# Kernel tuning notes

Measured on AMD Instinct MI355X. Metric: run time of the kernel, lower is better.

Reference implementation:

```python
import jax, jax.numpy as jnp
import numpy as np

N_NODES = 100000
N_EDGES = 3200000
N_GRAPHS = 256
DIMS = [38, 64, 32, 16]


def setup_inputs() -> dict:
    key = jax.random.key(0)
    ks = jax.random.split(key, 16)
    x = jax.random.normal(ks[0], (N_NODES, DIMS[0]), dtype=jnp.float32)
    edge_index = jax.random.randint(ks[1], (2, N_EDGES), 0, N_NODES, dtype=jnp.int64)
    batch_vec = jnp.sort(jax.random.randint(ks[2], (N_NODES,), 0, N_GRAPHS, dtype=jnp.int64))
    inp = {"x": x, "edge_index": edge_index, "batch_vec": batch_vec}
    # Per layer l: W_rel [out,in] (with bias b [out]), W_root [out,in] (no bias)
    ki = 3
    for l in range(3):
        din, dout = DIMS[l], DIMS[l + 1]
        s = 1.0 / np.sqrt(din)
        inp[f"W_rel{l}"] = jax.random.uniform(ks[ki], (dout, din), minval=-s, maxval=s, dtype=jnp.float32); ki += 1
        inp[f"b{l}"] = jax.random.uniform(ks[ki], (dout,), minval=-s, maxval=s, dtype=jnp.float32); ki += 1
        inp[f"W_root{l}"] = jax.random.uniform(ks[ki], (dout, din), minval=-s, maxval=s, dtype=jnp.float32); ki += 1
    return inp


def _graph_conv(x, src, dst, W_rel, b, W_root):
    # sum_{j -> i} x_j, then linear (equivalent to summing transformed messages)
    agg = jax.ops.segment_sum(x[src], dst, num_segments=N_NODES)  # [N, din]
    return agg @ W_rel.T + b + x @ W_root.T


def reference(x, edge_index, batch_vec, W_rel0, b0, W_root0, W_rel1, b1, W_root1, W_rel2, b2, W_root2):
    src, dst = edge_index[0], edge_index[1]
    h = jnp.tanh(_graph_conv(x, src, dst, W_rel0, b0, W_root0))
    h = jnp.tanh(_graph_conv(h, src, dst, W_rel1, b1, W_root1))
    h = _graph_conv(h, src, dst, W_rel2, b2, W_root2)
    # global mean pool over graphs
    sums = jax.ops.segment_sum(h, batch_vec, num_segments=N_GRAPHS)  # [G, 16]
    counts = jax.ops.segment_sum(jnp.ones((N_NODES,), dtype=h.dtype), batch_vec, num_segments=N_GRAPHS)
    pooled = sums / jnp.maximum(counts, 1.0)[:, None]
    return jnp.tanh(pooled)
```

## Files before the change

kernel.cpp:

```cpp
#include <hip/hip_runtime.h>
#include <math.h>

#define N_NODES  100000
#define N_EDGES  3200000
#define N_GRAPHS 256


#define BSHIFT 8
#define NB 391
#define CAP 10240
#define NBLK 320
#define EPB ((N_EDGES + NBLK - 1) / NBLK)

typedef _Float16 f16;
typedef _Float16 f16x2 __attribute__((ext_vector_type(2)));

__device__ __forceinline__ float fast_tanh(float x) {
    x = fminf(20.f, fmaxf(-20.f, x));
    float e = __expf(2.f * x);
    return (e - 1.f) / (e + 1.f);
}

__device__ __forceinline__ unsigned int pack_bf2(float a, float b) {
    unsigned int ua = __float_as_uint(a);
    unsigned int ub = __float_as_uint(b);
    ua += 0x7fffu + ((ua >> 16) & 1u);
    ub += 0x7fffu + ((ub >> 16) & 1u);
    return (ua >> 16) | (ub & 0xffff0000u);
}

__device__ __forceinline__ f16x2 u2h(unsigned int u) { union { unsigned int u; f16x2 h; } c; c.u = u; return c.h; }
__device__ __forceinline__ unsigned int h2u(f16x2 h) { union { unsigned int u; f16x2 h; } c; c.h = h; return c.u; }
__device__ __forceinline__ unsigned int mkh2(float a, float b) {
    f16x2 v; v.x = (f16)a; v.y = (f16)b; return h2u(v);
}

__device__ __forceinline__ float fdot2f(f16x2 a, f16x2 b, float c) {
#if __has_builtin(__builtin_amdgcn_fdot2)
    return __builtin_amdgcn_fdot2(a, b, c, false);
#else
    return c + (float)a.x * (float)b.x + (float)a.y * (float)b.y;
#endif
}

__global__ __launch_bounds__(256) void k_scatter2(const int* __restrict__ src,
                                                  const int* __restrict__ dst,
                                                  int* __restrict__ bucket_cnt,
                                                  int* __restrict__ ebuf) {
    __shared__ int hist[NB];
    __shared__ int base[NB];
    __shared__ int cur[NB];
    int tid = threadIdx.x, b = blockIdx.x;
    for (int i = tid; i < NB; i += 256) { hist[i] = 0; cur[i] = 0; }
    __syncthreads();
    int lo = b * EPB, hi = min(lo + EPB, N_EDGES);
    for (int e = lo + tid; e < hi; e += 256)
        atomicAdd(&hist[((unsigned int)dst[e]) >> BSHIFT], 1);
    __syncthreads();
    for (int i = tid; i < NB; i += 256) {
        int c = hist[i];
        base[i] = (c > 0) ? atomicAdd(&bucket_cnt[i], c) : 0;
    }
    __syncthreads();
    for (int e = lo + tid; e < hi; e += 256) {
        int d = dst[e];
        int bin = d >> BSHIFT;
        int r = base[bin] + atomicAdd(&cur[bin], 1);
        if (r < CAP) ebuf[bin * CAP + r] = src[e] | ((d & 255) << 17);
    }
}

__global__ __launch_bounds__(256) void k_bucket_csr2(const int* __restrict__ bucket_cnt,
                                                     int* __restrict__ ebuf,
                                                     int* __restrict__ rowptr,
                                                     int* __restrict__ rowend) {
    __shared__ int stage[CAP];
    __shared__ int cnt[256];
    __shared__ int off[256];
    __shared__ int cur[256];
    __shared__ int sscan[256];
    int b = blockIdx.x;
    int tid = threadIdx.x;
    int base = b * CAP;
    int n = min(bucket_cnt[b], CAP);
    cnt[tid] = 0;
    cur[tid] = 0;
    __syncthreads();
    for (int j = tid; j < n; j += 256) {
        int w = ebuf[base + j];
        stage[j] = w;
        atomicAdd(&cnt[((unsigned int)w) >> 17], 1);
    }
    __syncthreads();
    int v = cnt[tid];
    int val = v;
    sscan[tid] = val;
    __syncthreads();
#pragma unroll
    for (int o = 1; o < 256; o <<= 1) {
        int t = (tid >= o) ? sscan[tid - o] : 0;
        __syncthreads();
        val += t;
        sscan[tid] = val;
        __syncthreads();
    }
    int excl = val - v;
    off[tid] = excl;
    int node = (b << BSHIFT) + tid;
    if (node < N_NODES) {
        rowptr[node] = base + excl;
        rowend[node] = base + val;
    }
    __syncthreads();
    for (int j = tid; j < n; j += 256) {
        int w = stage[j];
        int dl = ((unsigned int)w) >> 17;
        int r = atomicAdd(&cur[dl], 1);
        ebuf[base + off[dl] + r] = w & 0x1FFFF;
    }
}

__global__ __launch_bounds__(256) void k_cast_slices(const float* __restrict__ in,
                                                     unsigned int* __restrict__ s0,
                                                     unsigned int* __restrict__ s1,
                                                     unsigned int* __restrict__ s2) {
    int i = blockIdx.x * 256 + threadIdx.x;
    if (i >= N_NODES * 19) return;
    int n = i / 19;
    int p = i - n * 19;
    float2 v = ((const float2*)in)[i];
    unsigned int w = pack_bf2(v.x, v.y);
    if (p < 8)       s0[n * 8 + p] = w;
    else if (p < 16) s1[n * 8 + p - 8] = w;
    else             s2[n * 3 + p - 16] = w;
}

template<int DIM2, int ASTRIDE, int OFF>
__global__ __launch_bounds__(256) void k_gather_slice(const unsigned int* __restrict__ feat,
                                                      const int* __restrict__ rowptr,
                                                      const int* __restrict__ rowend,
                                                      const int* __restrict__ elist,
                                                      float* __restrict__ agg) {
    int idx = blockIdx.x * 256 + threadIdx.x;
    if (idx >= N_NODES * DIM2) return;
    int n = idx / DIM2;
    int p = idx - n * DIM2;
    int j = rowptr[n];
    int e = rowend[n];
    float a0 = 0.f, a1 = 0.f;
    for (; j + 3 < e; j += 4) {
        int s0 = elist[j];
        int s1 = elist[j + 1];
        int s2 = elist[j + 2];
        int s3 = elist[j + 3];
        unsigned int w0 = feat[s0 * DIM2 + p];
        unsigned int w1 = feat[s1 * DIM2 + p];
        unsigned int w2 = feat[s2 * DIM2 + p];
        unsigned int w3 = feat[s3 * DIM2 + p];
        a0 += __uint_as_float(w0 << 16);
        a1 += __uint_as_float(w0 & 0xffff0000u);
        a0 += __uint_as_float(w1 << 16);
        a1 += __uint_as_float(w1 & 0xffff0000u);
        a0 += __uint_as_float(w2 << 16);
        a1 += __uint_as_float(w2 & 0xffff0000u);
        a0 += __uint_as_float(w3 << 16);
        a1 += __uint_as_float(w3 & 0xffff0000u);
    }
    for (; j < e; ++j) {
        unsigned int w = feat[elist[j] * DIM2 + p];
        a0 += __uint_as_float(w << 16);
        a1 += __uint_as_float(w & 0xffff0000u);
    }
    agg[n * ASTRIDE + OFF + 2 * p]     = a0;
    agg[n * ASTRIDE + OFF + 2 * p + 1] = a1;
}

__global__ __launch_bounds__(256) void k_fused0(const float* __restrict__ agg,
                                                const float* __restrict__ x,
                                                const float* __restrict__ Wrel0,
                                                const float* __restrict__ b0,
                                                const float* __restrict__ Wroot0,
                                                const float* __restrict__ Wrel1,
                                                const float* __restrict__ b1,
                                                const float* __restrict__ Wroot1,
                                                unsigned int* __restrict__ y1b0,
                                                unsigned int* __restrict__ y1b1,
                                                float* __restrict__ r1) {
    __shared__ unsigned int sWr[64 * 20];
    __shared__ unsigned int sWt[64 * 20];
    __shared__ unsigned int sW1r[32 * 32];
    __shared__ unsigned int sW1t[32 * 32];
    __shared__ float sb0[64];
    __shared__ float sb1[32];
    int tid = threadIdx.x;
    for (int i = tid; i < 64 * 20; i += 256) {
        int o = i / 20, d = i - o * 20;
        float a0 = (2 * d     < 38) ? Wrel0[o * 38 + 2 * d]     : 0.f;
        float a1 = (2 * d + 1 < 38) ? Wrel0[o * 38 + 2 * d + 1] : 0.f;
        float t0 = (2 * d     < 38) ? Wroot0[o * 38 + 2 * d]     : 0.f;
        float t1 = (2 * d + 1 < 38) ? Wroot0[o * 38 + 2 * d + 1] : 0.f;
        sWr[i] = mkh2(a0, a1);
        sWt[i] = mkh2(t0, t1);
    }
    for (int i = tid; i < 32 * 32; i += 256) {
        int op = i >> 5, j = i & 31;
        sW1r[i] = mkh2(Wrel1[j * 64 + 2 * op], Wrel1[j * 64 + 2 * op + 1]);
        sW1t[i] = mkh2(Wroot1[j * 64 + 2 * op], Wroot1[j * 64 + 2 * op + 1]);
    }
    if (tid < 64) sb0[tid] = b0[tid];
    if (tid < 32) sb1[tid] = b1[tid];
    __syncthreads();

    int lane = tid & 63;
    int ph = lane & 31;
    int sh = lane >> 5;
    int n0 = blockIdx.x * 256 + (tid >> 6) * 64 + 2 * ph;
    if (n0 >= N_NODES) return;
    int n1 = n0 + 1;

    unsigned int xa0[20], xx0[20], xa1[20], xx1[20];
    {
        const float2* A0 = (const float2*)(agg + (size_t)n0 * 38);
        const float2* X0 = (const float2*)(x   + (size_t)n0 * 38);
        const float2* A1 = (const float2*)(agg + (size_t)n1 * 38);
        const float2* X1 = (const float2*)(x   + (size_t)n1 * 38);
#pragma unroll
        for (int i = 0; i < 19; ++i) {
            float2 v;
            v = A0[i]; xa0[i] = mkh2(v.x, v.y);
            v = X0[i]; xx0[i] = mkh2(v.x, v.y);
            v = A1[i]; xa1[i] = mkh2(v.x, v.y);
            v = X1[i]; xx1[i] = mkh2(v.x, v.y);
        }
        xa0[19] = 0; xx0[19] = 0; xa1[19] = 0; xx1[19] = 0;
    }

    unsigned int hp0[16], hp1[16];
    int obase = sh * 32;
#pragma unroll
    for (int i = 0; i < 16; ++i) {
        float h00 = 0.f, h01 = 0.f, h10 = 0.f, h11 = 0.f;
#pragma unroll
        for (int par = 0; par < 2; ++par) {
            int o = obase + 2 * i + par;
            float c0 = sb0[o], c1 = 0.f, c2 = 0.f, c3 = 0.f;
            float d0 = sb0[o], d1 = 0.f, d2 = 0.f, d3 = 0.f;
            const uint4* wr = (const uint4*)(sWr + o * 20);
            const uint4* wt = (const uint4*)(sWt + o * 20);
#pragma unroll
            for (int q = 0; q < 5; ++q) {
                uint4 w = wr[q];
                c0 = fdot2f(u2h(xa0[4 * q + 0]), u2h(w.x), c0);
                c1 = fdot2f(u2h(xa0[4 * q + 1]), u2h(w.y), c1);
                c2 = fdot2f(u2h(xa0[4 * q + 2]), u2h(w.z), c2);
                c3 = fdot2f(u2h(xa0[4 * q + 3]), u2h(w.w), c3);
                d0 = fdot2f(u2h(xa1[4 * q + 0]), u2h(w.x), d0);
                d1 = fdot2f(u2h(xa1[4 * q + 1]), u2h(w.y), d1);
                d2 = fdot2f(u2h(xa1[4 * q + 2]), u2h(w.z), d2);
                d3 = fdot2f(u2h(xa1[4 * q + 3]), u2h(w.w), d3);
                uint4 v = wt[q];
                c0 = fdot2f(u2h(xx0[4 * q + 0]), u2h(v.x), c0);
                c1 = fdot2f(u2h(xx0[4 * q + 1]), u2h(v.y), c1);
                c2 = fdot2f(u2h(xx0[4 * q + 2]), u2h(v.z), c2);
                c3 = fdot2f(u2h(xx0[4 * q + 3]), u2h(v.w), c3);
                d0 = fdot2f(u2h(xx1[4 * q + 0]), u2h(v.x), d0);
                d1 = fdot2f(u2h(xx1[4 * q + 1]), u2h(v.y), d1);
                d2 = fdot2f(u2h(xx1[4 * q + 2]), u2h(v.z), d2);
                d3 = fdot2f(u2h(xx1[4 * q + 3]), u2h(v.w), d3);
            }
            float hA = fast_tanh(c0 + c1 + c2 + c3);
            float hB = fast_tanh(d0 + d1 + d2 + d3);
            if (par == 0) { h00 = hA; h10 = hB; }
            else          { h01 = hA; h11 = hB; }
        }
        hp0[i] = mkh2(h00, h01);
        hp1[i] = mkh2(h10, h11);
    }

    unsigned int H0[32], H1[32];
#pragma unroll
    for (int i = 0; i < 16; ++i) {
        unsigned int g0 = (unsigned int)__shfl_xor((int)hp0[i], 32);
        unsigned int g1 = (unsigned int)__shfl_xor((int)hp1[i], 32);
        if (sh == 0) { H0[i] = hp0[i]; H0[16 + i] = g0; H1[i] = hp1[i]; H1[16 + i] = g1; }
        else         { H0[i] = g0; H0[16 + i] = hp0[i]; H1[i] = g1; H1[16 + i] = hp1[i]; }
    }

    int jb = sh * 16;
    float y0[16], r0[16], y1v[16], r1v[16];
#pragma unroll
    for (int j = 0; j < 16; ++j) {
        y0[j] = 0.f; y1v[j] = 0.f;
        float bb = sb1[jb + j];
        r0[j] = bb; r1v[j] = bb;
    }
#pragma unroll
    for (int op = 0; op < 32; ++op) {
        f16x2 h0 = u2h(H0[op]);
        f16x2 h1 = u2h(H1[op]);
        const uint4* w1 = (const uint4*)(sW1r + op * 32 + jb);
        const uint4* w2 = (const uint4*)(sW1t + op * 32 + jb);
#pragma unroll
        for (int q = 0; q < 4; ++q) {
            uint4 a = w1[q], b = w2[q];
            y0[4 * q + 0] = fdot2f(h0, u2h(a.x), y0[4 * q + 0]);
            y0[4 * q + 1] = fdot2f(h0, u2h(a.y), y0[4 * q + 1]);
            y0[4 * q + 2] = fdot2f(h0, u2h(a.z), y0[4 * q + 2]);
            y0[4 * q + 3] = fdot2f(h0, u2h(a.w), y0[4 * q + 3]);
            y1v[4 * q + 0] = fdot2f(h1, u2h(a.x), y1v[4 * q + 0]);
            y1v[4 * q + 1] = fdot2f(h1, u2h(a.y), y1v[4 * q + 1]);
            y1v[4 * q + 2] = fdot2f(h1, u2h(a.z), y1v[4 * q + 2]);
            y1v[4 * q + 3] = fdot2f(h1, u2h(a.w), y1v[4 * q + 3]);
            r0[4 * q + 0] = fdot2f(h0, u2h(b.x), r0[4 * q + 0]);
            r0[4 * q + 1] = fdot2f(h0, u2h(b.y), r0[4 * q + 1]);
            r0[4 * q + 2] = fdot2f(h0, u2h(b.z), r0[4 * q + 2]);
            r0[4 * q + 3] = fdot2f(h0, u2h(b.w), r0[4 * q + 3]);
            r1v[4 * q + 0] = fdot2f(h1, u2h(b.x), r1v[4 * q + 0]);
            r1v[4 * q + 1] = fdot2f(h1, u2h(b.y), r1v[4 * q + 1]);
            r1v[4 * q + 2] = fdot2f(h1, u2h(b.z), r1v[4 * q + 2]);
            r1v[4 * q + 3] = fdot2f(h1, u2h(b.w), r1v[4 * q + 3]);
        }
    }

    unsigned int* yo0 = (sh ? y1b1 : y1b0) + (size_t)n0 * 8;
    unsigned int* yo1 = (sh ? y1b1 : y1b0) + (size_t)n1 * 8;
#pragma unroll
    for (int p = 0; p < 8; ++p) {
        yo0[p] = pack_bf2(y0[2 * p], y0[2 * p + 1]);
        yo1[p] = pack_bf2(y1v[2 * p], y1v[2 * p + 1]);
    }
    float4* ro0 = (float4*)(r1 + (size_t)n0 * 32 + jb);
    float4* ro1 = (float4*)(r1 + (size_t)n1 * 32 + jb);
#pragma unroll
    for (int q = 0; q < 4; ++q) {
        ro0[q] = make_float4(r0[4 * q], r0[4 * q + 1], r0[4 * q + 2], r0[4 * q + 3]);
        ro1[q] = make_float4(r1v[4 * q], r1v[4 * q + 1], r1v[4 * q + 2], r1v[4 * q + 3]);
    }
}

__global__ __launch_bounds__(256) void k_fused1(const float* __restrict__ agg,
                                                const float* __restrict__ r1,
                                                const float* __restrict__ Wrel2,
                                                float* __restrict__ h2,
                                                unsigned int* __restrict__ y2b)
{
    __shared__ float sW[32 * 16];
    int tid = threadIdx.x;
    for (int i = tid; i < 512; i += 256) {
        int k = i >> 4, j = i & 15;
        sW[i] = Wrel2[j * 32 + k];
    }
    __syncthreads();
    int n = blockIdx.x * 256 + tid;
    if (n >= N_NODES) return;
    const float4* a4 = (const float4*)(agg + (size_t)n * 32);
    const float4* r4 = (const float4*)(r1 + (size_t)n * 32);
    float h[32];
#pragma unroll
    for (int i = 0; i < 8; ++i) {
        float4 a = a4[i], r = r4[i];
        h[4 * i]     = fast_tanh(a.x + r.x);
        h[4 * i + 1] = fast_tanh(a.y + r.y);
        h[4 * i + 2] = fast_tanh(a.z + r.z);
        h[4 * i + 3] = fast_tanh(a.w + r.w);
    }
    float4* ho = (float4*)(h2 + (size_t)n * 32);
#pragma unroll
    for (int i = 0; i < 8; ++i) ho[i] = make_float4(h[4 * i], h[4 * i + 1], h[4 * i + 2], h[4 * i + 3]);
    float y[16];
#pragma unroll
    for (int j = 0; j < 16; ++j) y[j] = 0.f;
#pragma unroll
    for (int k = 0; k < 32; ++k) {
        const float4* w = (const float4*)(sW + k * 16);
#pragma unroll
        for (int j = 0; j < 4; ++j) {
            float4 wv = w[j];
            y[4 * j]     += h[k] * wv.x; y[4 * j + 1] += h[k] * wv.y;
            y[4 * j + 2] += h[k] * wv.z; y[4 * j + 3] += h[k] * wv.w;
        }
    }
    unsigned int* yo = y2b + (size_t)n * 8;
#pragma unroll
    for (int p = 0; p < 8; ++p) yo[p] = pack_bf2(y[2 * p], y[2 * p + 1]);
}

__global__ __launch_bounds__(256) void k_graph_start(const int* __restrict__ batch,
                                                     int* __restrict__ gstart) {
    int i = blockIdx.x * 256 + threadIdx.x;
    if (i >= N_NODES) return;
    int g = batch[i];
    int gp = (i == 0) ? -1 : batch[i - 1];
    for (int gg = gp + 1; gg <= g; ++gg) gstart[gg] = i;
    if (i == N_NODES - 1)
        for (int gg = g + 1; gg <= N_GRAPHS; ++gg) gstart[gg] = N_NODES;
}

__global__ __launch_bounds__(256) void k_pool(const float* __restrict__ agg,
                                              const float* __restrict__ h2,
                                              const int* __restrict__ gstart,
                                              float* __restrict__ psum)
{
    __shared__ float part[4][48];
    int g = blockIdx.x;
    int wave = threadIdx.x >> 6;
    int lane = threadIdx.x & 63;
    int s = gstart[g], e = gstart[g + 1];
    if (lane < 48) {
        float a0 = 0.f, a1 = 0.f;
        if (lane < 16) {
            int n = s + wave;
            for (; n + 4 < e; n += 8) {
                a0 += agg[n * 16 + lane];
                a1 += agg[(n + 4) * 16 + lane];
            }
            if (n < e) a0 += agg[n * 16 + lane];
        } else {
            int d = lane - 16;
            int n = s + wave;
            for (; n + 4 < e; n += 8) {
                a0 += h2[n * 32 + d];
                a1 += h2[(n + 4) * 32 + d];
            }
            if (n < e) a0 += h2[n * 32 + d];
        }
        part[wave][lane] = a0 + a1;
    }
    __syncthreads();
    if (threadIdx.x < 48)
        psum[g * 48 + threadIdx.x] = part[0][threadIdx.x] + part[1][threadIdx.x]
                                   + part[2][threadIdx.x] + part[3][threadIdx.x];
}

__global__ __launch_bounds__(256) void k_finalize2(const float* __restrict__ psum,
                                                   const float* __restrict__ Wroot,
                                                   const float* __restrict__ b,
                                                   const int* __restrict__ gstart,
                                                   float* __restrict__ out) {
    __shared__ float sW[16 * 32];
    __shared__ float sb[16];
    int tid = threadIdx.x;
    for (int i = tid; i < 16 * 32; i += 256) sW[i] = Wroot[i];
    if (tid < 16) sb[tid] = b[tid];
    __syncthreads();
    int idx = blockIdx.x * 256 + tid;
    if (idx >= N_GRAPHS * 16) return;
    int g = idx >> 4;
    int o = idx & 15;
    float cnt = (float)(gstart[g + 1] - gstart[g]);
    const float* p = psum + g * 48;
    float acc = p[o] + cnt * sb[o];
#pragma unroll
    for (int k = 0; k < 32; ++k) acc += p[16 + k] * sW[o * 32 + k];
    out[idx] = fast_tanh(acc / fmaxf(cnt, 1.f));
}

extern "C" void kernel_launch(void* const* d_in, const int* in_sizes, int n_in,
                              void* d_out, int out_size, void* d_ws, size_t ws_size,
                              hipStream_t stream) {
    const float* x      = (const float*)d_in[0];
    const int*   eidx   = (const int*)d_in[1];
    const int*   src    = eidx;
    const int*   dst    = eidx + N_EDGES;
    const int*   batch  = (const int*)d_in[2];
    const float* Wrel0  = (const float*)d_in[3];
    const float* b0     = (const float*)d_in[4];
    const float* Wroot0 = (const float*)d_in[5];
    const float* Wrel1  = (const float*)d_in[6];
    const float* b1     = (const float*)d_in[7];
    const float* Wroot1 = (const float*)d_in[8];
    const float* Wrel2  = (const float*)d_in[9];
    const float* b2     = (const float*)d_in[10];
    const float* Wroot2 = (const float*)d_in[11];
    float* out = (float*)d_out;

    float* ws   = (float*)d_ws;
    float* agg  = ws;
    float* r1   = agg + (size_t)N_NODES * 38;
    float* h2   = r1  + (size_t)N_NODES * 32;
    unsigned int* ybuf = (unsigned int*)(h2 + (size_t)N_NODES * 32);
    float* psum = (float*)(ybuf + (size_t)N_NODES * 16);
    int* rowptr      = (int*)(psum + N_GRAPHS * 48);
    int* rowend      = rowptr + N_NODES;
    int* gstart      = rowend + N_NODES;
    int* bucket_cnt  = gstart + 260;
    int* ebuf        = bucket_cnt + 400;
    unsigned int* xb0 = (unsigned int*)r1;
    unsigned int* xb1 = xb0 + (size_t)N_NODES * 8;
    unsigned int* xb2 = xb1 + (size_t)N_NODES * 8;
    unsigned int* y1b0 = ybuf;
    unsigned int* y1b1 = ybuf + (size_t)N_NODES * 8;
    unsigned int* y2b  = ybuf;

    k_cast_slices<<<(N_NODES * 19 + 255) / 256, 256, 0, stream>>>(x, xb0, xb1, xb2);

    hipMemsetAsync(bucket_cnt, 0, sizeof(int) * NB, stream);
    k_scatter2<<<NBLK, 256, 0, stream>>>(src, dst, bucket_cnt, ebuf);
    k_bucket_csr2<<<NB, 256, 0, stream>>>(bucket_cnt, ebuf, rowptr, rowend);
    k_graph_start<<<(N_NODES + 255) / 256, 256, 0, stream>>>(batch, gstart);

    k_gather_slice<8, 38, 0 ><<<(N_NODES * 8 + 255) / 256, 256, 0, stream>>>(xb0, rowptr, rowend, ebuf, agg);
    k_gather_slice<8, 38, 16><<<(N_NODES * 8 + 255) / 256, 256, 0, stream>>>(xb1, rowptr, rowend, ebuf, agg);
    k_gather_slice<3, 38, 32><<<(N_NODES * 3 + 255) / 256, 256, 0, stream>>>(xb2, rowptr, rowend, ebuf, agg);
    k_fused0<<<(N_NODES + 255) / 256, 256, 0, stream>>>(agg, x, Wrel0, b0, Wroot0,
                                                        Wrel1, b1, Wroot1, y1b0, y1b1, r1);

    k_gather_slice<8, 32, 0 ><<<(N_NODES * 8 + 255) / 256, 256, 0, stream>>>(y1b0, rowptr, rowend, ebuf, agg);
    k_gather_slice<8, 32, 16><<<(N_NODES * 8 + 255) / 256, 256, 0, stream>>>(y1b1, rowptr, rowend, ebuf, agg);
    k_fused1<<<(N_NODES + 255) / 256, 256, 0, stream>>>(agg, r1, Wrel2, h2, y2b);

    k_gather_slice<8, 16, 0 ><<<(N_NODES * 8 + 255) / 256, 256, 0, stream>>>(y2b, rowptr, rowend, ebuf, agg);

    k_pool<<<N_GRAPHS, 256, 0, stream>>>(agg, h2, gstart, psum);
    k_finalize2<<<(N_GRAPHS * 16 + 255) / 256, 256, 0, stream>>>(psum, Wroot2, b2, gstart, out);
}
```

Before: 349.8 us.

## Gather padded bf16 rows with 16-byte vector loads in single kernels per layer

Replaces the per-word sliced feature buffers and multiple gather launches with one padded, interleaved bf16 row layout, so each thread loads four packed words (eight features) per neighbor with one uint4 load. Layer 0 features are padded to 20 words and aggregates to a stride of 40. This cuts the number of gather kernels and edge-list re-reads, while giving each thread more accumulators and fewer threads overall. The scatter block count is also doubled.

```diff
diff --git a/kernel.cpp b/kernel.cpp
--- a/kernel.cpp
+++ b/kernel.cpp
@@ -9,7 +9,7 @@
 #define BSHIFT 8
 #define NB 391
 #define CAP 10240
-#define NBLK 320
+#define NBLK 640
 #define EPB ((N_EDGES + NBLK - 1) / NBLK)
 
 typedef _Float16 f16;
@@ -120,59 +120,70 @@
     }
 }
 
-__global__ __launch_bounds__(256) void k_cast_slices(const float* __restrict__ in,
-                                                     unsigned int* __restrict__ s0,
-                                                     unsigned int* __restrict__ s1,
-                                                     unsigned int* __restrict__ s2) {
+__global__ __launch_bounds__(256) void k_cast_pad(const float* __restrict__ in,
+                                                  unsigned int* __restrict__ out) {
     int i = blockIdx.x * 256 + threadIdx.x;
-    if (i >= N_NODES * 19) return;
-    int n = i / 19;
-    int p = i - n * 19;
-    float2 v = ((const float2*)in)[i];
-    unsigned int w = pack_bf2(v.x, v.y);
-    if (p < 8)       s0[n * 8 + p] = w;
-    else if (p < 16) s1[n * 8 + p - 8] = w;
-    else             s2[n * 3 + p - 16] = w;
-}
-
-template<int DIM2, int ASTRIDE, int OFF>
-__global__ __launch_bounds__(256) void k_gather_slice(const unsigned int* __restrict__ feat,
-                                                      const int* __restrict__ rowptr,
-                                                      const int* __restrict__ rowend,
-                                                      const int* __restrict__ elist,
-                                                      float* __restrict__ agg) {
+    if (i >= N_NODES * 20) return;
+    int n = i / 20;
+    int p = i - n * 20;
+    unsigned int w = 0;
+    if (p < 19) {
+        float2 v = ((const float2*)in)[n * 19 + p];
+        w = pack_bf2(v.x, v.y);
+    }
+    out[i] = w;
+}
+
+template<int NQ, int RSTRIDE, int ASTRIDE>
+__global__ __launch_bounds__(256) void k_gather_quad(const unsigned int* __restrict__ feat,
+                                                     const int* __restrict__ rowptr,
+                                                     const int* __restrict__ rowend,
+                                                     const int* __restrict__ elist,
+                                                     float* __restrict__ agg) {
     int idx = blockIdx.x * 256 + threadIdx.x;
-    if (idx >= N_NODES * DIM2) return;
-    int n = idx / DIM2;
-    int p = idx - n * DIM2;
+    if (idx >= N_NODES * NQ) return;
+    int n = idx / NQ;
+    int q = idx - n * NQ;
     int j = rowptr[n];
     int e = rowend[n];
-    float a0 = 0.f, a1 = 0.f;
-    for (; j + 3 < e; j += 4) {
+    const unsigned int* fq = feat + q * 4;
+    float a0 = 0.f, a1 = 0.f, a2 = 0.f, a3 = 0.f, a4 = 0.f, a5 = 0.f, a6 = 0.f, a7 = 0.f;
+    for (; j + 1 < e; j += 2) {
         int s0 = elist[j];
         int s1 = elist[j + 1];
-        int s2 = elist[j + 2];
-        int s3 = elist[j + 3];
-        unsigned int w0 = feat[s0 * DIM2 + p];
-        unsigned int w1 = feat[s1 * DIM2 + p];
-        unsigned int w2 = feat[s2 * DIM2 + p];
-        unsigned int w3 = feat[s3 * DIM2 + p];
-        a0 += __uint_as_float(w0 << 16);
-        a1 += __uint_as_float(w0 & 0xffff0000u);
-        a0 += __uint_as_float(w1 << 16);
-        a1 += __uint_as_float(w1 & 0xffff0000u);
-        a0 += __uint_as_float(w2 << 16);
-        a1 += __uint_as_float(w2 & 0xffff0000u);
-        a0 += __uint_as_float(w3 << 16);
-        a1 += __uint_as_float(w3 & 0xffff0000u);
-    }
-    for (; j < e; ++j) {
-        unsigned int w = feat[elist[j] * DIM2 + p];
-        a0 += __uint_as_float(w << 16);
-        a1 += __uint_as_float(w & 0xffff0000u);
-    }
-    agg[n * ASTRIDE + OFF + 2 * p]     = a0;
-    agg[n * ASTRIDE + OFF + 2 * p + 1] = a1;
+        uint4 w0 = *(const uint4*)(fq + (size_t)s0 * RSTRIDE);
+        uint4 w1 = *(const uint4*)(fq + (size_t)s1 * RSTRIDE);
+        a0 += __uint_as_float(w0.x << 16);
+        a1 += __uint_as_float(w0.x & 0xffff0000u);
+        a2 += __uint_as_float(w0.y << 16);
+        a3 += __uint_as_float(w0.y & 0xffff0000u);
+        a4 += __uint_as_float(w0.z << 16);
+        a5 += __uint_as_float(w0.z & 0xffff0000u);
+        a6 += __uint_as_float(w0.w << 16);
+        a7 += __uint_as_float(w0.w & 0xffff0000u);
+        a0 += __uint_as_float(w1.x << 16);
+        a1 += __uint_as_float(w1.x & 0xffff0000u);
+        a2 += __uint_as_float(w1.y << 16);
+        a3 += __uint_as_float(w1.y & 0xffff0000u);
+        a4 += __uint_as_float(w1.z << 16);
+        a5 += __uint_as_float(w1.z & 0xffff0000u);
+        a6 += __uint_as_float(w1.w << 16);
+        a7 += __uint_as_float(w1.w & 0xffff0000u);
+    }
+    if (j < e) {
+        uint4 w = *(const uint4*)(fq + (size_t)elist[j] * RSTRIDE);
+        a0 += __uint_as_float(w.x << 16);
+        a1 += __uint_as_float(w.x & 0xffff0000u);
+        a2 += __uint_as_float(w.y << 16);
+        a3 += __uint_as_float(w.y & 0xffff0000u);
+        a4 += __uint_as_float(w.z << 16);
+        a5 += __uint_as_float(w.z & 0xffff0000u);
+        a6 += __uint_as_float(w.w << 16);
+        a7 += __uint_as_float(w.w & 0xffff0000u);
+    }
+    float4* ao = (float4*)(agg + (size_t)n * ASTRIDE + q * 8);
+    ao[0] = make_float4(a0, a1, a2, a3);
+    ao[1] = make_float4(a4, a5, a6, a7);
 }
 
 __global__ __launch_bounds__(256) void k_fused0(const float* __restrict__ agg,
@@ -183,8 +194,7 @@
                                                 const float* __restrict__ Wrel1,
                                                 const float* __restrict__ b1,
                                                 const float* __restrict__ Wroot1,
-                                                unsigned int* __restrict__ y1b0,
-                                                unsigned int* __restrict__ y1b1,
+                                                unsigned int* __restrict__ y1b,
                                                 float* __restrict__ r1) {
     __shared__ unsigned int sWr[64 * 20];
     __shared__ unsigned int sWt[64 * 20];
@@ -220,9 +230,9 @@
 
     unsigned int xa0[20], xx0[20], xa1[20], xx1[20];
     {
-        const float2* A0 = (const float2*)(agg + (size_t)n0 * 38);
+        const float2* A0 = (const float2*)(agg + (size_t)n0 * 40);
         const float2* X0 = (const float2*)(x   + (size_t)n0 * 38);
-        const float2* A1 = (const float2*)(agg + (size_t)n1 * 38);
+        const float2* A1 = (const float2*)(agg + (size_t)n1 * 40);
         const float2* X1 = (const float2*)(x   + (size_t)n1 * 38);
 #pragma unroll
         for (int i = 0; i < 19; ++i) {
@@ -322,8 +332,8 @@
         }
     }
 
-    unsigned int* yo0 = (sh ? y1b1 : y1b0) + (size_t)n0 * 8;
-    unsigned int* yo1 = (sh ? y1b1 : y1b0) + (size_t)n1 * 8;
+    unsigned int* yo0 = y1b + (size_t)n0 * 16 + 8 * sh;
+    unsigned int* yo1 = y1b + (size_t)n1 * 16 + 8 * sh;
 #pragma unroll
     for (int p = 0; p < 8; ++p) {
         yo0[p] = pack_bf2(y0[2 * p], y0[2 * p + 1]);
@@ -476,7 +486,7 @@
 
     float* ws   = (float*)d_ws;
     float* agg  = ws;
-    float* r1   = agg + (size_t)N_NODES * 38;
+    float* r1   = agg + (size_t)N_NODES * 40;
     float* h2   = r1  + (size_t)N_NODES * 32;
     unsigned int* ybuf = (unsigned int*)(h2 + (size_t)N_NODES * 32);
     float* psum = (float*)(ybuf + (size_t)N_NODES * 16);
@@ -485,31 +495,25 @@
     int* gstart      = rowend + N_NODES;
     int* bucket_cnt  = gstart + 260;
     int* ebuf        = bucket_cnt + 400;
-    unsigned int* xb0 = (unsigned int*)r1;
-    unsigned int* xb1 = xb0 + (size_t)N_NODES * 8;
-    unsigned int* xb2 = xb1 + (size_t)N_NODES * 8;
-    unsigned int* y1b0 = ybuf;
-    unsigned int* y1b1 = ybuf + (size_t)N_NODES * 8;
-    unsigned int* y2b  = ybuf;
-
-    k_cast_slices<<<(N_NODES * 19 + 255) / 256, 256, 0, stream>>>(x, xb0, xb1, xb2);
+    unsigned int* xb = (unsigned int*)r1;
+    unsigned int* y1b = ybuf;
+    unsigned int* y2b = ybuf;
+
+    k_cast_pad<<<(N_NODES * 20 + 255) / 256, 256, 0, stream>>>(x, xb);
 
     hipMemsetAsync(bucket_cnt, 0, sizeof(int) * NB, stream);
     k_scatter2<<<NBLK, 256, 0, stream>>>(src, dst, bucket_cnt, ebuf);
     k_bucket_csr2<<<NB, 256, 0, stream>>>(bucket_cnt, ebuf, rowptr, rowend);
     k_graph_start<<<(N_NODES + 255) / 256, 256, 0, stream>>>(batch, gstart);
 
-    k_gather_slice<8, 38, 0 ><<<(N_NODES * 8 + 255) / 256, 256, 0, stream>>>(xb0, rowptr, rowend, ebuf, agg);
-    k_gather_slice<8, 38, 16><<<(N_NODES * 8 + 255) / 256, 256, 0, stream>>>(xb1, rowptr, rowend, ebuf, agg);
-    k_gather_slice<3, 38, 32><<<(N_NODES * 3 + 255) / 256, 256, 0, stream>>>(xb2, rowptr, rowend, ebuf, agg);
+    k_gather_quad<5, 20, 40><<<(N_NODES * 5 + 255) / 256, 256, 0, stream>>>(xb, rowptr, rowend, ebuf, agg);
     k_fused0<<<(N_NODES + 255) / 256, 256, 0, stream>>>(agg, x, Wrel0, b0, Wroot0,
-                                                        Wrel1, b1, Wroot1, y1b0, y1b1, r1);
-
-    k_gather_slice<8, 32, 0 ><<<(N_NODES * 8 + 255) / 256, 256, 0, stream>>>(y1b0, rowptr, rowend, ebuf, agg);
-    k_gather_slice<8, 32, 16><<<(N_NODES * 8 + 255) / 256, 256, 0, stream>>>(y1b1, rowptr, rowend, ebuf, agg);
+                                                        Wrel1, b1, Wroot1, y1b, r1);
+
+    k_gather_quad<4, 16, 32><<<(N_NODES * 4 + 255) / 256, 256, 0, stream>>>(y1b, rowptr, rowend, ebuf, agg);
     k_fused1<<<(N_NODES + 255) / 256, 256, 0, stream>>>(agg, r1, Wrel2, h2, y2b);
 
-    k_gather_slice<8, 16, 0 ><<<(N_NODES * 8 + 255) / 256, 256, 0, stream>>>(y2b, rowptr, rowend, ebuf, agg);
+    k_gather_quad<2, 8, 16><<<(N_NODES * 2 + 255) / 256, 256, 0, stream>>>(y2b, rowptr, rowend, ebuf, agg);
 
     k_pool<<<N_GRAPHS, 256, 0, stream>>>(agg, h2, gstart, psum);
     k_finalize2<<<(N_GRAPHS * 16 + 255) / 256, 256, 0, stream>>>(psum, Wroot2, b2, gstart, out);
```

After: 347.2 us. Within noise of the previous version (-0.7%).
